# Performance work log

Hardware: AMD Instinct MI355X
Metric: run time of the kernel (lower is better)

## Reference

```python
import jax, jax.numpy as jnp
import numpy as np

# LAB normalization constants (Zhang et al. colorization convention used in this repo)
L_CENT, L_NORM, AB_NORM = 50.0, 100.0, 110.0
_RGB2XYZ = np.array([[0.412453, 0.357580, 0.180423],
                     [0.212671, 0.715160, 0.072169],
                     [0.019334, 0.119193, 0.950227]], dtype=np.float32)
_XYZ_WHITE = np.array([0.95047, 1.0, 1.08883], dtype=np.float32)


def rgb2lab(rgb):
    """rgb: (B,3,H,W) in [-0.5,0.5] -> normalized LAB (B,3,H,W)."""
    rgb01 = rgb + 0.5  # [0,1]
    # sRGB gamma expansion (safe-where for grad stability)
    m = rgb01 > 0.04045
    rgb_safe = jnp.where(m, rgb01, 1.0)
    lin = jnp.where(m, ((rgb_safe + 0.055) / 1.055) ** 2.4, rgb01 / 12.92)
    xyz = jnp.einsum('ij,bjhw->bihw', jnp.asarray(_RGB2XYZ), lin)
    xyz = xyz / jnp.asarray(_XYZ_WHITE)[None, :, None, None]
    m2 = xyz > 0.008856
    xyz_safe = jnp.where(m2, xyz, 1.0)
    f = jnp.where(m2, xyz_safe ** (1.0 / 3.0), 7.787 * xyz + 16.0 / 116.0)
    L = 116.0 * f[:, 1] - 16.0
    a = 500.0 * (f[:, 0] - f[:, 1])
    b = 200.0 * (f[:, 1] - f[:, 2])
    return jnp.stack([(L - L_CENT) / L_NORM, a / AB_NORM, b / AB_NORM], axis=1)


def setup_inputs() -> dict:
    key = jax.random.key(0)
    k0, k1, k2, k3 = jax.random.split(key, 4)
    B, C, H, W, F = 2, 3, 64, 64, 64
    rgb0 = jax.random.uniform(k0, (B, C, H, W), dtype=jnp.float32) - 0.5
    rgb1 = jax.random.uniform(k1, (B, C, H, W), dtype=jnp.float32) - 0.5
    feat0 = jax.random.normal(k2, (B, F, H, W), dtype=jnp.float32)
    feat1 = jax.random.normal(k3, (B, F, H, W), dtype=jnp.float32)
    return {"rgb0": rgb0, "rgb1": rgb1, "feat0": feat0, "feat1": feat1}


def reference(rgb0, rgb1, feat0, feat1):
    l1_coeff, huber_coeff = 1.0, 1.0  # hyp.col2D_l1_coeff / hyp.col2D_huber_coeff
    B, C, H, W = rgb0.shape
    F = feat0.shape[1]
    N = H * W
    lab0 = rgb2lab(rgb0)
    lab1 = rgb2lab(rgb1)
    f0 = feat0.reshape(B, F, N)
    f1 = feat1.reshape(B, F, N)
    corr = jnp.einsum('bfn,bfm->bnm', f0, f1) / 0.07  # (B,N,N)
    att = jax.nn.softmax(corr, axis=2)
    lab1_flat = lab1.reshape(B, C, N)
    # broadcast-multiply-sum in the original == attention @ labels (same math)
    lab0_e = jnp.einsum('bnm,bcm->bcn', att, lab1_flat).reshape(B, C, H, W)
    diff = lab0_e - lab0
    l1_loss = jnp.mean(jnp.sum(jnp.abs(diff), axis=1, keepdims=True))
    ad = jnp.abs(diff)
    huber = jnp.where(ad < 1.0, 0.5 * ad * ad, ad - 0.5)  # SmoothL1, beta=1
    huber_loss = jnp.mean(jnp.sum(huber, axis=1, keepdims=True))
    total_loss = l1_coeff * l1_loss + huber_coeff * huber_loss
    return total_loss
```

## Files before the change

kernel.cpp:

```cpp
#include <hip/hip_runtime.h>
#include <math.h>

#define NPIX   4096
#define FDIM   64
#define BATCH  2
#define SPLIT  16
#define CHUNK  (NPIX / SPLIT)
#define NTILE  (CHUNK / 16)

typedef __attribute__((ext_vector_type(8))) short short8;
typedef __attribute__((ext_vector_type(4))) float floatx4;

__device__ __forceinline__ float exp2f_(float x) { return __builtin_amdgcn_exp2f(x); }

__device__ __forceinline__ short f2bf(float x) {
    union { float f; unsigned u; } c; c.f = x;
    unsigned r = (c.u + 0x7FFFu + ((c.u >> 16) & 1u)) >> 16;
    return (short)r;
}

__device__ __forceinline__ float gamma_expand(float u) {
    return u > 0.04045f ? powf((u + 0.055f) * (1.0f / 1.055f), 2.4f)
                        : u * (1.0f / 12.92f);
}
__device__ __forceinline__ float lab_f(float t) {
    return t > 0.008856f ? cbrtf(t) : 7.787f * t + (16.0f / 116.0f);
}

__global__ __launch_bounds__(256) void prep_kernel(
    const float* __restrict__ rgb0, const float* __restrict__ rgb1,
    const float* __restrict__ feat0, const float* __restrict__ feat1,
    float* __restrict__ lab0, float* __restrict__ lab1,
    short* __restrict__ f0t, short* __restrict__ f1t,
    float* __restrict__ out)
{
    int bid = blockIdx.x;
    int tid = threadIdx.x;

    if (bid < 256) {
        __shared__ short Tsm[64 * 72];
        int pair = bid >> 6;
        int tensor = pair >> 1;
        int bb = pair & 1;
        int n0 = (bid & 63) * 64;
        const float* src = (tensor ? feat1 : feat0) + (size_t)bb * FDIM * NPIX;
        short* dst = (tensor ? f1t : f0t) + (size_t)bb * NPIX * FDIM;
        float scale = tensor ? 1.0f : (1.442695040888963f / 0.07f);

        int f = tid >> 2;
        int slot = tid & 3;
        #pragma unroll
        for (int i = 0; i < 4; ++i) {
            int col4 = slot * 4 + i;
            int noff = col4 * 4;
            float4 v = *(const float4*)&src[(size_t)f * NPIX + n0 + noff];
            Tsm[(noff + 0) * 72 + f] = f2bf(v.x * scale);
            Tsm[(noff + 1) * 72 + f] = f2bf(v.y * scale);
            Tsm[(noff + 2) * 72 + f] = f2bf(v.z * scale);
            Tsm[(noff + 3) * 72 + f] = f2bf(v.w * scale);
        }
        __syncthreads();
        #pragma unroll
        for (int i = 0; i < 2; ++i) {
            int idx = i * 256 + tid;
            int row = idx >> 3, ch = idx & 7;
            *(short8*)&dst[(size_t)(n0 + row) * FDIM + ch * 8] =
                *(const short8*)&Tsm[row * 72 + ch * 8];
        }
        return;
    }

    if (bid == 256 && tid == 0) out[0] = 0.0f;

    int gid = (bid - 256) * 256 + tid;
    int img = gid / (BATCH * NPIX);
    int rem = gid - img * (BATCH * NPIX);
    int b = rem / NPIX;
    int n = rem - b * NPIX;
    const float* rgb = img ? rgb1 : rgb0;
    float* lab = img ? lab1 : lab0;

    size_t i0 = (size_t)(b * 3 + 0) * NPIX + n;
    size_t i1 = (size_t)(b * 3 + 1) * NPIX + n;
    size_t i2 = (size_t)(b * 3 + 2) * NPIX + n;

    float r = gamma_expand(rgb[i0] + 0.5f);
    float g = gamma_expand(rgb[i1] + 0.5f);
    float bl = gamma_expand(rgb[i2] + 0.5f);

    float X = (0.412453f * r + 0.357580f * g + 0.180423f * bl) * (1.0f / 0.95047f);
    float Y = (0.212671f * r + 0.715160f * g + 0.072169f * bl);
    float Z = (0.019334f * r + 0.119193f * g + 0.950227f * bl) * (1.0f / 1.08883f);

    float fx = lab_f(X), fy = lab_f(Y), fz = lab_f(Z);
    float L = 116.0f * fy - 16.0f;
    float a = 500.0f * (fx - fy);
    float bb2 = 200.0f * (fy - fz);

    lab[i0] = (L - 50.0f) * (1.0f / 100.0f);
    lab[i1] = a * (1.0f / 110.0f);
    lab[i2] = bb2 * (1.0f / 110.0f);
}

__global__ __launch_bounds__(256, 4) void attn_kernel(
    const short* __restrict__ f0t, const short* __restrict__ f1t,
    const float* __restrict__ lab1ws, float* __restrict__ partials)
{
    int bid = blockIdx.x;
    int rowblk = bid & 31;
    int chunk = (bid >> 5) & (SPLIT - 1);
    int b = bid >> 9;
    int tid = threadIdx.x;
    int w = tid >> 6;
    int l = tid & 63;
    int c = l & 15;
    int q = l >> 4;

    int n_base = rowblk * 128 + w * 32;
    int m_base = chunk * CHUNK;

    const short8* yp0 = (const short8*)(f0t + ((size_t)b * NPIX + n_base + c) * FDIM + q * 8);
    short8 y0a = yp0[0], y0b = yp0[4];
    const short8* yp1 = (const short8*)(f0t + ((size_t)b * NPIX + n_base + 16 + c) * FDIM + q * 8);
    short8 y1a = yp1[0], y1b = yp1[4];

    const short8* xbase = (const short8*)(f1t + ((size_t)b * NPIX + m_base + c) * FDIM + q * 8);
    const float* labA = lab1ws + (size_t)(b * 3 + 0) * NPIX + m_base + q * 4;
    const float* labB = lab1ws + (size_t)(b * 3 + 1) * NPIX + m_base + q * 4;
    const float* labC = lab1ws + (size_t)(b * 3 + 2) * NPIX + m_base + q * 4;

    float m0s = -INFINITY, sum0 = 0.0f, a0A = 0.0f, a0B = 0.0f, a0C = 0.0f;
    float m1s = -INFINITY, sum1 = 0.0f, a1A = 0.0f, a1B = 0.0f, a1C = 0.0f;

    short8 xa = xbase[0], xb = xbase[4];
    float4 lA = *(const float4*)labA;
    float4 lB = *(const float4*)labB;
    float4 lC = *(const float4*)labC;

    #pragma unroll
    for (int t = 0; t < NTILE; ++t) {
        short8 xa_n, xb_n;
        float4 lA_n, lB_n, lC_n;
        if (t + 1 < NTILE) {
            const short8* xp = xbase + (size_t)(t + 1) * 128;
            xa_n = xp[0];
            xb_n = xp[4];
            lA_n = *(const float4*)(labA + (t + 1) * 16);
            lB_n = *(const float4*)(labB + (t + 1) * 16);
            lC_n = *(const float4*)(labC + (t + 1) * 16);
        }

        floatx4 z = (floatx4)(0.0f);
        floatx4 acc0 = __builtin_amdgcn_mfma_f32_16x16x32_bf16(xa, y0a, z, 0, 0, 0);
        acc0 = __builtin_amdgcn_mfma_f32_16x16x32_bf16(xb, y0b, acc0, 0, 0, 0);
        floatx4 acc1 = __builtin_amdgcn_mfma_f32_16x16x32_bf16(xa, y1a, z, 0, 0, 0);
        acc1 = __builtin_amdgcn_mfma_f32_16x16x32_bf16(xb, y1b, acc1, 0, 0, 0);

        {
            float L0 = acc0[0], L1 = acc0[1], L2 = acc0[2], L3 = acc0[3];
            float tmax = fmaxf(fmaxf(L0, L1), fmaxf(L2, L3));
            float nm = fmaxf(m0s, tmax);
            float sc = exp2f_(m0s - nm);
            float p0 = exp2f_(L0 - nm);
            float p1 = exp2f_(L1 - nm);
            float p2 = exp2f_(L2 - nm);
            float p3 = exp2f_(L3 - nm);
            sum0 = sum0 * sc + ((p0 + p1) + (p2 + p3));
            a0A = a0A * sc + ((p0 * lA.x + p1 * lA.y) + (p2 * lA.z + p3 * lA.w));
            a0B = a0B * sc + ((p0 * lB.x + p1 * lB.y) + (p2 * lB.z + p3 * lB.w));
            a0C = a0C * sc + ((p0 * lC.x + p1 * lC.y) + (p2 * lC.z + p3 * lC.w));
            m0s = nm;
        }
        {
            float L0 = acc1[0], L1 = acc1[1], L2 = acc1[2], L3 = acc1[3];
            float tmax = fmaxf(fmaxf(L0, L1), fmaxf(L2, L3));
            float nm = fmaxf(m1s, tmax);
            float sc = exp2f_(m1s - nm);
            float p0 = exp2f_(L0 - nm);
            float p1 = exp2f_(L1 - nm);
            float p2 = exp2f_(L2 - nm);
            float p3 = exp2f_(L3 - nm);
            sum1 = sum1 * sc + ((p0 + p1) + (p2 + p3));
            a1A = a1A * sc + ((p0 * lA.x + p1 * lA.y) + (p2 * lA.z + p3 * lA.w));
            a1B = a1B * sc + ((p0 * lB.x + p1 * lB.y) + (p2 * lB.z + p3 * lB.w));
            a1C = a1C * sc + ((p0 * lC.x + p1 * lC.y) + (p2 * lC.z + p3 * lC.w));
            m1s = nm;
        }

        if (t + 1 < NTILE) {
            xa = xa_n; xb = xb_n;
            lA = lA_n; lB = lB_n; lC = lC_n;
        }
    }

    #pragma unroll
    for (int mask = 16; mask <= 32; mask <<= 1) {
        {
            float om = __shfl_xor(m0s, mask, 64);
            float os = __shfl_xor(sum0, mask, 64);
            float oA = __shfl_xor(a0A, mask, 64);
            float oB = __shfl_xor(a0B, mask, 64);
            float oC = __shfl_xor(a0C, mask, 64);
            float nm = fmaxf(m0s, om);
            float w1 = exp2f_(m0s - nm);
            float w2 = exp2f_(om - nm);
            sum0 = sum0 * w1 + os * w2;
            a0A = a0A * w1 + oA * w2;
            a0B = a0B * w1 + oB * w2;
            a0C = a0C * w1 + oC * w2;
            m0s = nm;
        }
        {
            float om = __shfl_xor(m1s, mask, 64);
            float os = __shfl_xor(sum1, mask, 64);
            float oA = __shfl_xor(a1A, mask, 64);
            float oB = __shfl_xor(a1B, mask, 64);
            float oC = __shfl_xor(a1C, mask, 64);
            float nm = fmaxf(m1s, om);
            float w1 = exp2f_(m1s - nm);
            float w2 = exp2f_(om - nm);
            sum1 = sum1 * w1 + os * w2;
            a1A = a1A * w1 + oA * w2;
            a1B = a1B * w1 + oB * w2;
            a1C = a1C * w1 + oC * w2;
            m1s = nm;
        }
    }

    if (q == 0) {
        size_t pbase = (size_t)(b * SPLIT + chunk) * 5 * NPIX;
        int n0 = n_base + c;
        partials[pbase + 0 * NPIX + n0] = m0s;
        partials[pbase + 1 * NPIX + n0] = sum0;
        partials[pbase + 2 * NPIX + n0] = a0A;
        partials[pbase + 3 * NPIX + n0] = a0B;
        partials[pbase + 4 * NPIX + n0] = a0C;
        int n1 = n_base + 16 + c;
        partials[pbase + 0 * NPIX + n1] = m1s;
        partials[pbase + 1 * NPIX + n1] = sum1;
        partials[pbase + 2 * NPIX + n1] = a1A;
        partials[pbase + 3 * NPIX + n1] = a1B;
        partials[pbase + 4 * NPIX + n1] = a1C;
    }
}

__global__ void loss_kernel(const float* __restrict__ partials,
                            const float* __restrict__ lab0ws,
                            float* __restrict__ out)
{
    int gid = blockIdx.x * blockDim.x + threadIdx.x;
    int b = gid >> 12;
    int n = gid & (NPIX - 1);

    float M = -INFINITY;
    #pragma unroll
    for (int ch = 0; ch < SPLIT; ++ch)
        M = fmaxf(M, partials[((size_t)(b * SPLIT + ch) * 5 + 0) * NPIX + n]);
    float S = 0.0f, A0 = 0.0f, A1 = 0.0f, A2 = 0.0f;
    #pragma unroll
    for (int ch = 0; ch < SPLIT; ++ch) {
        size_t base = (size_t)(b * SPLIT + ch) * 5 * NPIX + n;
        float w = exp2f_(partials[base + 0 * NPIX] - M);
        S  += partials[base + 1 * NPIX] * w;
        A0 += partials[base + 2 * NPIX] * w;
        A1 += partials[base + 3 * NPIX] * w;
        A2 += partials[base + 4 * NPIX] * w;
    }
    float inv_s = 1.0f / S;
    float d0 = A0 * inv_s - lab0ws[(size_t)(b * 3 + 0) * NPIX + n];
    float d1 = A1 * inv_s - lab0ws[(size_t)(b * 3 + 1) * NPIX + n];
    float d2 = A2 * inv_s - lab0ws[(size_t)(b * 3 + 2) * NPIX + n];

    float val = 0.0f;
    #pragma unroll
    for (int cc = 0; cc < 3; ++cc) {
        float d = (cc == 0) ? d0 : (cc == 1) ? d1 : d2;
        float ad = fabsf(d);
        float hub = (ad < 1.0f) ? 0.5f * ad * ad : ad - 0.5f;
        val += ad + hub;
    }

    #pragma unroll
    for (int off = 32; off > 0; off >>= 1)
        val += __shfl_down(val, off);

    __shared__ float wsum[4];
    int lane = threadIdx.x & 63;
    int wave = threadIdx.x >> 6;
    if (lane == 0) wsum[wave] = val;
    __syncthreads();
    if (threadIdx.x == 0) {
        float s = wsum[0] + wsum[1] + wsum[2] + wsum[3];
        atomicAdd(out, s * (1.0f / 8192.0f));
    }
}

extern "C" void kernel_launch(void* const* d_in, const int* in_sizes, int n_in,
                              void* d_out, int out_size, void* d_ws, size_t ws_size,
                              hipStream_t stream) {
    const float* rgb0  = (const float*)d_in[0];
    const float* rgb1  = (const float*)d_in[1];
    const float* feat0 = (const float*)d_in[2];
    const float* feat1 = (const float*)d_in[3];
    float* out = (float*)d_out;
    float* ws  = (float*)d_ws;

    float* lab0 = ws;
    float* lab1 = ws + 24576;
    float* partials = ws + 49152;
    short* f0t = (short*)(ws + 49152 + 655360);
    short* f1t = f0t + (size_t)BATCH * NPIX * FDIM;

    prep_kernel<<<320, 256, 0, stream>>>(rgb0, rgb1, feat0, feat1, lab0, lab1, f0t, f1t, out);

    int attn_grid = BATCH * SPLIT * 32;
    attn_kernel<<<attn_grid, 256, 0, stream>>>(f0t, f1t, lab1, partials);

    loss_kernel<<<(BATCH * NPIX) / 256, 256, 0, stream>>>(partials, lab0, out);
}
```

Measured before the change: 93.67 us.

## Stage lab chunk in LDS and deepen K-tile register prefetch to four

The lab values for the block's key chunk are loaded once per block into shared memory instead of being fetched from global memory by each wave every tile. The feature-tile prefetch becomes a 4-deep rotating register buffer, so global loads are issued further ahead of the MFMAs that use them. This is meant to hide global load latency in the streaming softmax loop. It costs more registers for the prefetch buffers, a __syncthreads, and LDS reads in the inner loop, and the outer loop is no longer fully unrolled.

```diff
diff --git a/kernel.cpp b/kernel.cpp
--- a/kernel.cpp
+++ b/kernel.cpp
@@ -106,6 +106,8 @@
     const short* __restrict__ f0t, const short* __restrict__ f1t,
     const float* __restrict__ lab1ws, float* __restrict__ partials)
 {
+    __shared__ float Lt[3 * CHUNK];
+
     int bid = blockIdx.x;
     int rowblk = bid & 31;
     int chunk = (bid >> 5) & (SPLIT - 1);
@@ -119,77 +121,82 @@
     int n_base = rowblk * 128 + w * 32;
     int m_base = chunk * CHUNK;
 
+    if (tid < 192) {
+        int cc = tid >> 6;
+        int m4 = tid & 63;
+        *(float4*)&Lt[cc * CHUNK + m4 * 4] =
+            *(const float4*)&lab1ws[(size_t)(b * 3 + cc) * NPIX + m_base + m4 * 4];
+    }
+
     const short8* yp0 = (const short8*)(f0t + ((size_t)b * NPIX + n_base + c) * FDIM + q * 8);
     short8 y0a = yp0[0], y0b = yp0[4];
     const short8* yp1 = (const short8*)(f0t + ((size_t)b * NPIX + n_base + 16 + c) * FDIM + q * 8);
     short8 y1a = yp1[0], y1b = yp1[4];
 
     const short8* xbase = (const short8*)(f1t + ((size_t)b * NPIX + m_base + c) * FDIM + q * 8);
-    const float* labA = lab1ws + (size_t)(b * 3 + 0) * NPIX + m_base + q * 4;
-    const float* labB = lab1ws + (size_t)(b * 3 + 1) * NPIX + m_base + q * 4;
-    const float* labC = lab1ws + (size_t)(b * 3 + 2) * NPIX + m_base + q * 4;
+
+    short8 xa_r[4], xb_r[4];
+    #pragma unroll
+    for (int i = 0; i < 4; ++i) {
+        xa_r[i] = xbase[(size_t)i * 128];
+        xb_r[i] = xbase[(size_t)i * 128 + 4];
+    }
+
+    __syncthreads();
 
     float m0s = -INFINITY, sum0 = 0.0f, a0A = 0.0f, a0B = 0.0f, a0C = 0.0f;
     float m1s = -INFINITY, sum1 = 0.0f, a1A = 0.0f, a1B = 0.0f, a1C = 0.0f;
 
-    short8 xa = xbase[0], xb = xbase[4];
-    float4 lA = *(const float4*)labA;
-    float4 lB = *(const float4*)labB;
-    float4 lC = *(const float4*)labC;
-
-    #pragma unroll
-    for (int t = 0; t < NTILE; ++t) {
-        short8 xa_n, xb_n;
-        float4 lA_n, lB_n, lC_n;
-        if (t + 1 < NTILE) {
-            const short8* xp = xbase + (size_t)(t + 1) * 128;
-            xa_n = xp[0];
-            xb_n = xp[4];
-            lA_n = *(const float4*)(labA + (t + 1) * 16);
-            lB_n = *(const float4*)(labB + (t + 1) * 16);
-            lC_n = *(const float4*)(labC + (t + 1) * 16);
-        }
-
-        floatx4 z = (floatx4)(0.0f);
-        floatx4 acc0 = __builtin_amdgcn_mfma_f32_16x16x32_bf16(xa, y0a, z, 0, 0, 0);
-        acc0 = __builtin_amdgcn_mfma_f32_16x16x32_bf16(xb, y0b, acc0, 0, 0, 0);
-        floatx4 acc1 = __builtin_amdgcn_mfma_f32_16x16x32_bf16(xa, y1a, z, 0, 0, 0);
-        acc1 = __builtin_amdgcn_mfma_f32_16x16x32_bf16(xb, y1b, acc1, 0, 0, 0);
-
-        {
-            float L0 = acc0[0], L1 = acc0[1], L2 = acc0[2], L3 = acc0[3];
-            float tmax = fmaxf(fmaxf(L0, L1), fmaxf(L2, L3));
-            float nm = fmaxf(m0s, tmax);
-            float sc = exp2f_(m0s - nm);
-            float p0 = exp2f_(L0 - nm);
-            float p1 = exp2f_(L1 - nm);
-            float p2 = exp2f_(L2 - nm);
-            float p3 = exp2f_(L3 - nm);
-            sum0 = sum0 * sc + ((p0 + p1) + (p2 + p3));
-            a0A = a0A * sc + ((p0 * lA.x + p1 * lA.y) + (p2 * lA.z + p3 * lA.w));
-            a0B = a0B * sc + ((p0 * lB.x + p1 * lB.y) + (p2 * lB.z + p3 * lB.w));
-            a0C = a0C * sc + ((p0 * lC.x + p1 * lC.y) + (p2 * lC.z + p3 * lC.w));
-            m0s = nm;
-        }
-        {
-            float L0 = acc1[0], L1 = acc1[1], L2 = acc1[2], L3 = acc1[3];
-            float tmax = fmaxf(fmaxf(L0, L1), fmaxf(L2, L3));
-            float nm = fmaxf(m1s, tmax);
-            float sc = exp2f_(m1s - nm);
-            float p0 = exp2f_(L0 - nm);
-            float p1 = exp2f_(L1 - nm);
-            float p2 = exp2f_(L2 - nm);
-            float p3 = exp2f_(L3 - nm);
-            sum1 = sum1 * sc + ((p0 + p1) + (p2 + p3));
-            a1A = a1A * sc + ((p0 * lA.x + p1 * lA.y) + (p2 * lA.z + p3 * lA.w));
-            a1B = a1B * sc + ((p0 * lB.x + p1 * lB.y) + (p2 * lB.z + p3 * lB.w));
-            a1C = a1C * sc + ((p0 * lC.x + p1 * lC.y) + (p2 * lC.z + p3 * lC.w));
-            m1s = nm;
-        }
-
-        if (t + 1 < NTILE) {
-            xa = xa_n; xb = xb_n;
-            lA = lA_n; lB = lB_n; lC = lC_n;
+    for (int tb = 0; tb < NTILE; tb += 4) {
+        #pragma unroll
+        for (int i = 0; i < 4; ++i) {
+            int t = tb + i;
+
+            floatx4 z = (floatx4)(0.0f);
+            floatx4 acc0 = __builtin_amdgcn_mfma_f32_16x16x32_bf16(xa_r[i], y0a, z, 0, 0, 0);
+            acc0 = __builtin_amdgcn_mfma_f32_16x16x32_bf16(xb_r[i], y0b, acc0, 0, 0, 0);
+            floatx4 acc1 = __builtin_amdgcn_mfma_f32_16x16x32_bf16(xa_r[i], y1a, z, 0, 0, 0);
+            acc1 = __builtin_amdgcn_mfma_f32_16x16x32_bf16(xb_r[i], y1b, acc1, 0, 0, 0);
+
+            if (t + 4 < NTILE) {
+                xa_r[i] = xbase[(size_t)(t + 4) * 128];
+                xb_r[i] = xbase[(size_t)(t + 4) * 128 + 4];
+            }
+
+            float4 lA = *(const float4*)&Lt[0 * CHUNK + t * 16 + q * 4];
+            float4 lB = *(const float4*)&Lt[1 * CHUNK + t * 16 + q * 4];
+            float4 lC = *(const float4*)&Lt[2 * CHUNK + t * 16 + q * 4];
+
+            {
+                float L0 = acc0[0], L1 = acc0[1], L2 = acc0[2], L3 = acc0[3];
+                float tmax = fmaxf(fmaxf(L0, L1), fmaxf(L2, L3));
+                float nm = fmaxf(m0s, tmax);
+                float sc = exp2f_(m0s - nm);
+                float p0 = exp2f_(L0 - nm);
+                float p1 = exp2f_(L1 - nm);
+                float p2 = exp2f_(L2 - nm);
+                float p3 = exp2f_(L3 - nm);
+                sum0 = sum0 * sc + ((p0 + p1) + (p2 + p3));
+                a0A = a0A * sc + ((p0 * lA.x + p1 * lA.y) + (p2 * lA.z + p3 * lA.w));
+                a0B = a0B * sc + ((p0 * lB.x + p1 * lB.y) + (p2 * lB.z + p3 * lB.w));
+                a0C = a0C * sc + ((p0 * lC.x + p1 * lC.y) + (p2 * lC.z + p3 * lC.w));
+                m0s = nm;
+            }
+            {
+                float L0 = acc1[0], L1 = acc1[1], L2 = acc1[2], L3 = acc1[3];
+                float tmax = fmaxf(fmaxf(L0, L1), fmaxf(L2, L3));
+                float nm = fmaxf(m1s, tmax);
+                float sc = exp2f_(m1s - nm);
+                float p0 = exp2f_(L0 - nm);
+                float p1 = exp2f_(L1 - nm);
+                float p2 = exp2f_(L2 - nm);
+                float p3 = exp2f_(L3 - nm);
+                sum1 = sum1 * sc + ((p0 + p1) + (p2 + p3));
+                a1A = a1A * sc + ((p0 * lA.x + p1 * lA.y) + (p2 * lA.z + p3 * lA.w));
+                a1B = a1B * sc + ((p0 * lB.x + p1 * lB.y) + (p2 * lB.z + p3 * lB.w));
+                a1C = a1C * sc + ((p0 * lC.x + p1 * lC.y) + (p2 * lC.z + p3 * lC.w));
+                m1s = nm;
+            }
         }
     }
 
```

Measured after the change: 88.80 us. 5.2% less time.

## Fuse feature transpose and LAB conversion into attention and loss kernels

Applied to the files above, without the earlier changes.

Removes the separate prep kernel. The attention kernel now loads fp32 features straight from the inputs, converts them to bf16 and transposes them through shared memory, and computes LAB for its chunk of rgb1 in shared memory. The loss kernel recomputes LAB for rgb0 inline. This drops one launch and the workspace round trip. In exchange each block redoes the transpose and conversion of its f0 and f1 tiles, which means redundant global reads (f1 is reloaded by 32 row blocks). The MFMA loop now reads from LDS instead of prefetching from global memory.

```diff
diff --git a/kernel.cpp b/kernel.cpp
--- a/kernel.cpp
+++ b/kernel.cpp
@@ -5,18 +5,23 @@
 #define FDIM   64
 #define BATCH  2
 #define SPLIT  16
-#define CHUNK  (NPIX / SPLIT)
+#define CHUNK  256
+#define BLKN   128
 #define NTILE  (CHUNK / 16)
+#define PITCH  72
 
 typedef __attribute__((ext_vector_type(8))) short short8;
 typedef __attribute__((ext_vector_type(4))) float floatx4;
 
 __device__ __forceinline__ float exp2f_(float x) { return __builtin_amdgcn_exp2f(x); }
 
-__device__ __forceinline__ short f2bf(float x) {
+__device__ __forceinline__ unsigned short f2bf(float x) {
     union { float f; unsigned u; } c; c.f = x;
     unsigned r = (c.u + 0x7FFFu + ((c.u >> 16) & 1u)) >> 16;
-    return (short)r;
+    return (unsigned short)r;
+}
+__device__ __forceinline__ unsigned pk_bf(float lo, float hi) {
+    return (unsigned)f2bf(lo) | ((unsigned)f2bf(hi) << 16);
 }
 
 __device__ __forceinline__ float gamma_expand(float u) {
@@ -26,135 +31,112 @@
 __device__ __forceinline__ float lab_f(float t) {
     return t > 0.008856f ? cbrtf(t) : 7.787f * t + (16.0f / 116.0f);
 }
-
-__global__ __launch_bounds__(256) void prep_kernel(
-    const float* __restrict__ rgb0, const float* __restrict__ rgb1,
-    const float* __restrict__ feat0, const float* __restrict__ feat1,
-    float* __restrict__ lab0, float* __restrict__ lab1,
-    short* __restrict__ f0t, short* __restrict__ f1t,
-    float* __restrict__ out)
-{
-    int bid = blockIdx.x;
-    int tid = threadIdx.x;
-
-    if (bid < 256) {
-        __shared__ short Tsm[64 * 72];
-        int pair = bid >> 6;
-        int tensor = pair >> 1;
-        int bb = pair & 1;
-        int n0 = (bid & 63) * 64;
-        const float* src = (tensor ? feat1 : feat0) + (size_t)bb * FDIM * NPIX;
-        short* dst = (tensor ? f1t : f0t) + (size_t)bb * NPIX * FDIM;
-        float scale = tensor ? 1.0f : (1.442695040888963f / 0.07f);
-
-        int f = tid >> 2;
-        int slot = tid & 3;
-        #pragma unroll
-        for (int i = 0; i < 4; ++i) {
-            int col4 = slot * 4 + i;
-            int noff = col4 * 4;
-            float4 v = *(const float4*)&src[(size_t)f * NPIX + n0 + noff];
-            Tsm[(noff + 0) * 72 + f] = f2bf(v.x * scale);
-            Tsm[(noff + 1) * 72 + f] = f2bf(v.y * scale);
-            Tsm[(noff + 2) * 72 + f] = f2bf(v.z * scale);
-            Tsm[(noff + 3) * 72 + f] = f2bf(v.w * scale);
-        }
-        __syncthreads();
-        #pragma unroll
-        for (int i = 0; i < 2; ++i) {
-            int idx = i * 256 + tid;
-            int row = idx >> 3, ch = idx & 7;
-            *(short8*)&dst[(size_t)(n0 + row) * FDIM + ch * 8] =
-                *(const short8*)&Tsm[row * 72 + ch * 8];
-        }
-        return;
-    }
-
-    if (bid == 256 && tid == 0) out[0] = 0.0f;
-
-    int gid = (bid - 256) * 256 + tid;
-    int img = gid / (BATCH * NPIX);
-    int rem = gid - img * (BATCH * NPIX);
-    int b = rem / NPIX;
-    int n = rem - b * NPIX;
-    const float* rgb = img ? rgb1 : rgb0;
-    float* lab = img ? lab1 : lab0;
-
-    size_t i0 = (size_t)(b * 3 + 0) * NPIX + n;
-    size_t i1 = (size_t)(b * 3 + 1) * NPIX + n;
-    size_t i2 = (size_t)(b * 3 + 2) * NPIX + n;
-
-    float r = gamma_expand(rgb[i0] + 0.5f);
-    float g = gamma_expand(rgb[i1] + 0.5f);
-    float bl = gamma_expand(rgb[i2] + 0.5f);
-
+__device__ __forceinline__ void rgb_to_lab(const float* rgb, size_t plane, size_t idx,
+                                           float& o0, float& o1, float& o2) {
+    float r  = gamma_expand(rgb[idx] + 0.5f);
+    float g  = gamma_expand(rgb[plane + idx] + 0.5f);
+    float bl = gamma_expand(rgb[2 * plane + idx] + 0.5f);
     float X = (0.412453f * r + 0.357580f * g + 0.180423f * bl) * (1.0f / 0.95047f);
     float Y = (0.212671f * r + 0.715160f * g + 0.072169f * bl);
     float Z = (0.019334f * r + 0.119193f * g + 0.950227f * bl) * (1.0f / 1.08883f);
-
     float fx = lab_f(X), fy = lab_f(Y), fz = lab_f(Z);
-    float L = 116.0f * fy - 16.0f;
-    float a = 500.0f * (fx - fy);
-    float bb2 = 200.0f * (fy - fz);
-
-    lab[i0] = (L - 50.0f) * (1.0f / 100.0f);
-    lab[i1] = a * (1.0f / 110.0f);
-    lab[i2] = bb2 * (1.0f / 110.0f);
+    o0 = (116.0f * fy - 16.0f - 50.0f) * (1.0f / 100.0f);
+    o1 = (500.0f * (fx - fy)) * (1.0f / 110.0f);
+    o2 = (200.0f * (fy - fz)) * (1.0f / 110.0f);
 }
 
 __global__ __launch_bounds__(256, 4) void attn_kernel(
-    const short* __restrict__ f0t, const short* __restrict__ f1t,
-    const float* __restrict__ lab1ws, float* __restrict__ partials)
+    const float* __restrict__ feat0, const float* __restrict__ feat1,
+    const float* __restrict__ rgb1, float* __restrict__ partials,
+    float* __restrict__ out)
 {
+    __shared__ short Sm[CHUNK * PITCH];
+    __shared__ float Lt[3 * CHUNK];
+
     int bid = blockIdx.x;
     int rowblk = bid & 31;
     int chunk = (bid >> 5) & (SPLIT - 1);
     int b = bid >> 9;
+    int n_blk = rowblk * BLKN;
+    int m_base = chunk * CHUNK;
+
     int tid = threadIdx.x;
     int w = tid >> 6;
     int l = tid & 63;
     int c = l & 15;
     int q = l >> 4;
 
-    int n_base = rowblk * 128 + w * 32;
-    int m_base = chunk * CHUNK;
-
-    const short8* yp0 = (const short8*)(f0t + ((size_t)b * NPIX + n_base + c) * FDIM + q * 8);
-    short8 y0a = yp0[0], y0b = yp0[4];
-    const short8* yp1 = (const short8*)(f0t + ((size_t)b * NPIX + n_base + 16 + c) * FDIM + q * 8);
-    short8 y1a = yp1[0], y1b = yp1[4];
-
-    const short8* xbase = (const short8*)(f1t + ((size_t)b * NPIX + m_base + c) * FDIM + q * 8);
-    const float* labA = lab1ws + (size_t)(b * 3 + 0) * NPIX + m_base + q * 4;
-    const float* labB = lab1ws + (size_t)(b * 3 + 1) * NPIX + m_base + q * 4;
-    const float* labC = lab1ws + (size_t)(b * 3 + 2) * NPIX + m_base + q * 4;
+    if (bid == 0 && tid == 0) out[0] = 0.0f;
+
+    unsigned* SmU = (unsigned*)Sm;
+    int p = tid >> 3;
+    int sub = tid & 7;
+
+    {
+        const float s = 1.442695040888963f / 0.07f;
+        const float* r0 = feat0 + ((size_t)b * FDIM + 2 * p) * NPIX + n_blk;
+        const float* r1 = r0 + NPIX;
+        #pragma unroll
+        for (int i = 0; i < BLKN / 32; ++i) {
+            int n0 = i * 32 + sub * 4;
+            float4 vA = *(const float4*)&r0[n0];
+            float4 vB = *(const float4*)&r1[n0];
+            SmU[(n0 + 0) * (PITCH / 2) + p] = pk_bf(vA.x * s, vB.x * s);
+            SmU[(n0 + 1) * (PITCH / 2) + p] = pk_bf(vA.y * s, vB.y * s);
+            SmU[(n0 + 2) * (PITCH / 2) + p] = pk_bf(vA.z * s, vB.z * s);
+            SmU[(n0 + 3) * (PITCH / 2) + p] = pk_bf(vA.w * s, vB.w * s);
+        }
+    }
+    __syncthreads();
+
+    int nl = w * 32 + c;
+    short8 y0a = *(const short8*)&Sm[nl * PITCH + q * 8];
+    short8 y0b = *(const short8*)&Sm[nl * PITCH + 32 + q * 8];
+    short8 y1a = *(const short8*)&Sm[(nl + 16) * PITCH + q * 8];
+    short8 y1b = *(const short8*)&Sm[(nl + 16) * PITCH + 32 + q * 8];
+    __syncthreads();
+
+    {
+        const float* r0 = feat1 + ((size_t)b * FDIM + 2 * p) * NPIX + m_base;
+        const float* r1 = r0 + NPIX;
+        #pragma unroll
+        for (int i = 0; i < CHUNK / 32; ++i) {
+            int m0 = i * 32 + sub * 4;
+            float4 vA = *(const float4*)&r0[m0];
+            float4 vB = *(const float4*)&r1[m0];
+            SmU[(m0 + 0) * (PITCH / 2) + p] = pk_bf(vA.x, vB.x);
+            SmU[(m0 + 1) * (PITCH / 2) + p] = pk_bf(vA.y, vB.y);
+            SmU[(m0 + 2) * (PITCH / 2) + p] = pk_bf(vA.z, vB.z);
+            SmU[(m0 + 3) * (PITCH / 2) + p] = pk_bf(vA.w, vB.w);
+        }
+    }
+    {
+        float o0, o1, o2;
+        rgb_to_lab(rgb1 + (size_t)b * 3 * NPIX, NPIX, (size_t)(m_base + tid), o0, o1, o2);
+        Lt[0 * CHUNK + tid] = o0;
+        Lt[1 * CHUNK + tid] = o1;
+        Lt[2 * CHUNK + tid] = o2;
+    }
+    __syncthreads();
 
     float m0s = -INFINITY, sum0 = 0.0f, a0A = 0.0f, a0B = 0.0f, a0C = 0.0f;
     float m1s = -INFINITY, sum1 = 0.0f, a1A = 0.0f, a1B = 0.0f, a1C = 0.0f;
 
-    short8 xa = xbase[0], xb = xbase[4];
-    float4 lA = *(const float4*)labA;
-    float4 lB = *(const float4*)labB;
-    float4 lC = *(const float4*)labC;
-
-    #pragma unroll
+    #pragma unroll 4
     for (int t = 0; t < NTILE; ++t) {
-        short8 xa_n, xb_n;
-        float4 lA_n, lB_n, lC_n;
-        if (t + 1 < NTILE) {
-            const short8* xp = xbase + (size_t)(t + 1) * 128;
-            xa_n = xp[0];
-            xb_n = xp[4];
-            lA_n = *(const float4*)(labA + (t + 1) * 16);
-            lB_n = *(const float4*)(labB + (t + 1) * 16);
-            lC_n = *(const float4*)(labC + (t + 1) * 16);
-        }
+        const short* xr = &Sm[(t * 16 + c) * PITCH + q * 8];
+        short8 xa = *(const short8*)xr;
+        short8 xb = *(const short8*)(xr + 32);
 
         floatx4 z = (floatx4)(0.0f);
         floatx4 acc0 = __builtin_amdgcn_mfma_f32_16x16x32_bf16(xa, y0a, z, 0, 0, 0);
         acc0 = __builtin_amdgcn_mfma_f32_16x16x32_bf16(xb, y0b, acc0, 0, 0, 0);
         floatx4 acc1 = __builtin_amdgcn_mfma_f32_16x16x32_bf16(xa, y1a, z, 0, 0, 0);
         acc1 = __builtin_amdgcn_mfma_f32_16x16x32_bf16(xb, y1b, acc1, 0, 0, 0);
+
+        float4 lA = *(const float4*)&Lt[0 * CHUNK + t * 16 + q * 4];
+        float4 lB = *(const float4*)&Lt[1 * CHUNK + t * 16 + q * 4];
+        float4 lC = *(const float4*)&Lt[2 * CHUNK + t * 16 + q * 4];
 
         {
             float L0 = acc0[0], L1 = acc0[1], L2 = acc0[2], L3 = acc0[3];
@@ -186,11 +168,6 @@
             a1C = a1C * sc + ((p0 * lC.x + p1 * lC.y) + (p2 * lC.z + p3 * lC.w));
             m1s = nm;
         }
-
-        if (t + 1 < NTILE) {
-            xa = xa_n; xb = xb_n;
-            lA = lA_n; lB = lB_n; lC = lC_n;
-        }
     }
 
     #pragma unroll
@@ -229,13 +206,13 @@
 
     if (q == 0) {
         size_t pbase = (size_t)(b * SPLIT + chunk) * 5 * NPIX;
-        int n0 = n_base + c;
+        int n0 = n_blk + w * 32 + c;
         partials[pbase + 0 * NPIX + n0] = m0s;
         partials[pbase + 1 * NPIX + n0] = sum0;
         partials[pbase + 2 * NPIX + n0] = a0A;
         partials[pbase + 3 * NPIX + n0] = a0B;
         partials[pbase + 4 * NPIX + n0] = a0C;
-        int n1 = n_base + 16 + c;
+        int n1 = n0 + 16;
         partials[pbase + 0 * NPIX + n1] = m1s;
         partials[pbase + 1 * NPIX + n1] = sum1;
         partials[pbase + 2 * NPIX + n1] = a1A;
@@ -245,7 +222,7 @@
 }
 
 __global__ void loss_kernel(const float* __restrict__ partials,
-                            const float* __restrict__ lab0ws,
+                            const float* __restrict__ rgb0,
                             float* __restrict__ out)
 {
     int gid = blockIdx.x * blockDim.x + threadIdx.x;
@@ -266,10 +243,13 @@
         A1 += partials[base + 3 * NPIX] * w;
         A2 += partials[base + 4 * NPIX] * w;
     }
+    float l0, l1, l2;
+    rgb_to_lab(rgb0 + (size_t)b * 3 * NPIX, NPIX, (size_t)n, l0, l1, l2);
+
     float inv_s = 1.0f / S;
-    float d0 = A0 * inv_s - lab0ws[(size_t)(b * 3 + 0) * NPIX + n];
-    float d1 = A1 * inv_s - lab0ws[(size_t)(b * 3 + 1) * NPIX + n];
-    float d2 = A2 * inv_s - lab0ws[(size_t)(b * 3 + 2) * NPIX + n];
+    float d0 = A0 * inv_s - l0;
+    float d1 = A1 * inv_s - l1;
+    float d2 = A2 * inv_s - l2;
 
     float val = 0.0f;
     #pragma unroll
@@ -303,18 +283,10 @@
     const float* feat0 = (const float*)d_in[2];
     const float* feat1 = (const float*)d_in[3];
     float* out = (float*)d_out;
-    float* ws  = (float*)d_ws;
-
-    float* lab0 = ws;
-    float* lab1 = ws + 24576;
-    float* partials = ws + 49152;
-    short* f0t = (short*)(ws + 49152 + 655360);
-    short* f1t = f0t + (size_t)BATCH * NPIX * FDIM;
-
-    prep_kernel<<<320, 256, 0, stream>>>(rgb0, rgb1, feat0, feat1, lab0, lab1, f0t, f1t, out);
-
-    int attn_grid = BATCH * SPLIT * 32;
-    attn_kernel<<<attn_grid, 256, 0, stream>>>(f0t, f1t, lab1, partials);
-
-    loss_kernel<<<(BATCH * NPIX) / 256, 256, 0, stream>>>(partials, lab0, out);
-}
+    float* partials = (float*)d_ws;
+
+    int attn_grid = BATCH * SPLIT * (NPIX / BLKN);
+    attn_kernel<<<attn_grid, 256, 0, stream>>>(feat0, feat1, rgb1, partials, out);
+
+    loss_kernel<<<(BATCH * NPIX) / 256, 256, 0, stream>>>(partials, rgb0, out);
+}
```

Measured after the change: 88.60 us. -5.4%, faster.
